# Kernel optimization log

Measured on AMD Instinct MI355X. Metric: run time of the kernel, lower is better.

The kernel has to match this reference:

```python
import jax, jax.numpy as jnp
import numpy as np

B, S, E, H = 2, 2048, 1024, 16
D = E // H  # head dim = 64
NEG_INF = -1e30


def alibi_slopes(n_head):
    # standard ALiBi slopes: 2^(-8*i/n_head), i = 1..n_head
    return jnp.asarray([2.0 ** (-8.0 * (i + 1) / n_head) for i in range(n_head)], dtype=jnp.float32)


def setup_inputs() -> dict:
    key = jax.random.key(0)
    ks = jax.random.split(key, 5)
    scale = 0.02
    return {
        "x": jax.random.normal(ks[0], (B, S, E), dtype=jnp.float32),
        "W_kqv": jax.random.normal(ks[1], (E, 3 * E), dtype=jnp.float32) * scale,
        "b_kqv": jnp.zeros((3 * E,), dtype=jnp.float32),
        "W_proj": jax.random.normal(ks[2], (E, E), dtype=jnp.float32) * scale,
        "b_proj": jnp.zeros((E,), dtype=jnp.float32),
        "slopes": alibi_slopes(H),
    }


def reference(x, W_kqv, b_kqv, W_proj, b_proj, slopes):
    b, s, e = x.shape
    kqv = x @ W_kqv + b_kqv                       # [b, s, 3e]
    k, q, v = jnp.split(kqv, 3, axis=-1)          # split order: k, q, v
    k = k.reshape(b, s, H, D)
    q = q.reshape(b, s, H, D)
    v = v.reshape(b, s, H, D)
    attn = jnp.einsum("bqhd,bkhd->bhqk", q, k) * (1.0 / jnp.sqrt(jnp.float32(D)))
    # ALiBi bias: slope_h * (j - i) for j <= i, -inf above diagonal (causal)
    i = jnp.arange(s)[:, None]
    j = jnp.arange(s)[None, :]
    rel = (j - i).astype(jnp.float32)             # [s, s]
    bias = slopes[:, None, None] * jnp.tril(rel)  # [h, s, s]
    bias = jnp.where(j > i, NEG_INF, bias)
    attn = jax.nn.softmax(attn + bias[None], axis=-1)
    # dropout is identity in eval mode
    y = jnp.einsum("bhqk,bkhd->bqhd", attn, v).reshape(b, s, e)
    return y @ W_proj + b_proj
```

## Files before the change

kernel.cpp:

```cpp
#include <hip/hip_runtime.h>

typedef unsigned short u16;
typedef float f32x4 __attribute__((ext_vector_type(4)));
typedef __bf16 bfx8 __attribute__((ext_vector_type(8)));
typedef __bf16 bfx4 __attribute__((ext_vector_type(4)));
typedef u16 u16x8 __attribute__((ext_vector_type(8)));
typedef u16 u16x4 __attribute__((ext_vector_type(4)));

#define B_ 2
#define S_ 2048
#define E_ 1024
#define H_ 16
#define D_ 64

__device__ __forceinline__ u16 f2bf(float f) {
  unsigned u = __float_as_uint(f);
  u = u + 0x7FFFu + ((u >> 16) & 1u);
  return (u16)(u >> 16);
}

__device__ __forceinline__ int swz128(int o) { return o ^ ((o >> 3) & 0x70); }

__device__ __forceinline__ void gload16(const void* g, void* l) {
  __builtin_amdgcn_global_load_lds((const __attribute__((address_space(1))) void*)g,
                                   (__attribute__((address_space(3))) void*)l, 16, 0, 0);
}

__device__ const signed char TQI[60] = {31, 31, 30, 30, 29, 29, 28, 28, 27, 27, 26, 26, 25, 25, 24,
                                        24, 23, 23, 22, 21, 20, 19, 18, 17, 16, 15, 14, 13, 12, 11,
                                        22, 10, 21, 9,  20, 8,  31, 19, 7,  30, 18, 6,  29, 17, 5,
                                        28, 16, 4,  27, 15, 3,  26, 14, 2,  25, 13, 1,  24, 12, 0};
__device__ const signed char TT0[60] = {0,  12, 0,  12, 0,  12, 0,  12, 0,  12, 0,  12, 0,  12, 0,
                                        12, 0,  12, 0,  0,  0,  0,  0,  0,  0,  0,  0,  0,  0,  0,
                                        12, 0,  12, 0,  12, 0,  24, 12, 0,  24, 12, 0,  24, 12, 0,
                                        24, 12, 0,  24, 12, 0,  24, 12, 0,  24, 12, 0,  24, 12, 0};
__device__ const signed char TT1[60] = {12, 24, 12, 24, 12, 24, 12, 24, 12, 24, 12, 24, 12, 24, 12,
                                        24, 12, 24, 12, 12, 12, 12, 12, 12, 12, 12, 12, 12, 12, 12,
                                        23, 11, 22, 10, 21, 9,  32, 20, 8,  31, 19, 7,  30, 18, 6,
                                        29, 17, 5,  28, 16, 4,  27, 15, 3,  26, 14, 2,  25, 13, 1};
__device__ const signed char TSL[60] = {45, 46, 42, 43, 39, 40, 36, 37, 33, 34, 30, 31, 27, 28, 24,
                                        25, 22, 23, 20, 18, 16, 14, 12, 10, 8,  6,  4,  2,  0,  -1,
                                        21, -1, 19, -1, 17, -1, 47, 15, -1, 44, 13, -1, 41, 11, -1,
                                        38, 9,  -1, 35, 7,  -1, 32, 5,  -1, 29, 3,  -1, 26, 1,  -1};

__global__ __launch_bounds__(256) void prep(const float* __restrict__ x,
                                            const float* __restrict__ Wk,
                                            const float* __restrict__ Wp, u16* __restrict__ xb,
                                            u16* __restrict__ wkt, u16* __restrict__ wpt) {
  __shared__ float tile[64][65];
  const int id = blockIdx.x, tid = threadIdx.x;
  if (id < 2048) {
    const float4* in4 = reinterpret_cast<const float4*>(x);
    u16x4* out4 = reinterpret_cast<u16x4*>(xb);
    int i = id * 256 + tid;
#pragma unroll
    for (int p = 0; p < 2; ++p, i += 524288) {
      const float4 v = in4[i];
      u16x4 o = {f2bf(v.x), f2bf(v.y), f2bf(v.z), f2bf(v.w)};
      out4[i] = o;
    }
    return;
  }
  const float* in;
  u16* out;
  int R, C, bx, by;
  if (id < 2816) {
    const int t = id - 2048;
    in = Wk; out = wkt; R = 1024; C = 3072; bx = t % 48; by = t / 48;
  } else {
    const int t = id - 2816;
    in = Wp; out = wpt; R = 1024; C = 1024; bx = t & 15; by = t >> 4;
  }
  const int ct = bx * 64, rt = by * 64;
#pragma unroll
  for (int p = 0; p < 4; ++p) {
    int f = p * 256 + tid;
    int row = f >> 4, c4 = (f & 15) << 2;
    const float4 v = *reinterpret_cast<const float4*>(in + (size_t)(rt + row) * C + ct + c4);
    tile[row][c4 + 0] = v.x; tile[row][c4 + 1] = v.y;
    tile[row][c4 + 2] = v.z; tile[row][c4 + 3] = v.w;
  }
  __syncthreads();
#pragma unroll
  for (int p = 0; p < 4; ++p) {
    int g = p * 256 + tid;
    int orow = g >> 4, k4 = (g & 15) << 2;
    u16x4 o = {f2bf(tile[k4 + 0][orow]), f2bf(tile[k4 + 1][orow]),
               f2bf(tile[k4 + 2][orow]), f2bf(tile[k4 + 3][orow])};
    *reinterpret_cast<u16x4*>(out + (size_t)(ct + orow) * R + rt + k4) = o;
  }
}

__global__ __launch_bounds__(256) void gemm_kqv(const u16* __restrict__ A,
                                                const u16* __restrict__ Bt,
                                                const float* __restrict__ bias, int M, int N, int K,
                                                u16* __restrict__ outK, u16* __restrict__ outQ,
                                                u16* __restrict__ outVt) {
  __shared__ __align__(16) u16 sA[128 * 64];
  __shared__ __align__(16) u16 sB[128 * 64];
  const int tid = threadIdx.x, lane = tid & 63;
  const int wave = tid >> 6, wr = wave >> 1, wc = wave & 1;
  int lin = blockIdx.y * gridDim.x + blockIdx.x;
  const int nwg = gridDim.x * gridDim.y;
  if ((nwg & 7) == 0) {
    const int cpx = nwg >> 3;
    lin = (lin & 7) * cpx + (lin >> 3);
  }
  const int bm = (lin / gridDim.x) * 128, bn = (lin % gridDim.x) * 128;
  const int r8 = lane >> 3, c16 = (lane & 7) ^ r8;
  f32x4 acc[4][4] = {};
  for (int k0 = 0; k0 < K; k0 += 64) {
#pragma unroll
    for (int i = 0; i < 4; ++i) {
      const int c = wave * 4 + i;
      const int row = c * 8 + r8;
      gload16(A + (size_t)(bm + row) * K + k0 + c16 * 8, (char*)sA + c * 1024);
      gload16(Bt + (size_t)(bn + row) * K + k0 + c16 * 8, (char*)sB + c * 1024);
    }
    __syncthreads();
#pragma unroll
    for (int kc = 0; kc < 2; ++kc) {
      bfx8 af[4], bf[4];
#pragma unroll
      for (int mf = 0; mf < 4; ++mf) {
        int o = swz128(((wr * 64 + mf * 16 + (lane & 15)) << 7) + kc * 64 + ((lane >> 4) << 4));
        af[mf] = *reinterpret_cast<const bfx8*>(reinterpret_cast<const char*>(sA) + o);
      }
#pragma unroll
      for (int nf = 0; nf < 4; ++nf) {
        int o = swz128(((wc * 64 + nf * 16 + (lane & 15)) << 7) + kc * 64 + ((lane >> 4) << 4));
        bf[nf] = *reinterpret_cast<const bfx8*>(reinterpret_cast<const char*>(sB) + o);
      }
#pragma unroll
      for (int mf = 0; mf < 4; ++mf)
#pragma unroll
        for (int nf = 0; nf < 4; ++nf)
          acc[mf][nf] = __builtin_amdgcn_mfma_f32_16x16x32_bf16(af[mf], bf[nf], acc[mf][nf], 0, 0, 0);
    }
    __syncthreads();
  }
#pragma unroll
  for (int mf = 0; mf < 4; ++mf)
#pragma unroll
    for (int nf = 0; nf < 4; ++nf)
#pragma unroll
      for (int r = 0; r < 4; ++r) {
        const int row = bm + wr * 64 + mf * 16 + ((lane >> 4) << 2) + r;
        const int col = bn + wc * 64 + nf * 16 + (lane & 15);
        const float v = acc[mf][nf][r] + bias[col];
        const int chunk = col >> 10, w = col & 1023, h = w >> 6, dd = w & 63;
        const int b = row >> 11, s = row & 2047;
        const int bh = b * H_ + h;
        if (chunk == 0)
          outK[((size_t)bh * S_ + s) * D_ + dd] = f2bf(v);
        else if (chunk == 1)
          outQ[((size_t)bh * S_ + s) * D_ + dd] = f2bf(v);
        else
          outVt[((size_t)bh * D_ + dd) * S_ + s] = f2bf(v);
      }
}

__global__ __launch_bounds__(512) void gemm_proj(const u16* __restrict__ A,
                                                 const u16* __restrict__ Bt,
                                                 const float* __restrict__ bias, int M, int N,
                                                 int K, float* __restrict__ outF) {
  __shared__ __align__(16) u16 sA[128 * 64];
  __shared__ __align__(16) u16 sB[128 * 64];
  const int tid = threadIdx.x, lane = tid & 63;
  const int wave = tid >> 6, wr = wave >> 2, wc = wave & 3;
  int lin = blockIdx.y * gridDim.x + blockIdx.x;
  const int nwg = gridDim.x * gridDim.y;
  if ((nwg & 7) == 0) {
    const int cpx = nwg >> 3;
    lin = (lin & 7) * cpx + (lin >> 3);
  }
  const int bm = (lin / gridDim.x) * 128, bn = (lin % gridDim.x) * 128;
  const int r8 = lane >> 3, c16 = (lane & 7) ^ r8;
  f32x4 acc[4][2] = {};
  for (int k0 = 0; k0 < K; k0 += 64) {
#pragma unroll
    for (int i = 0; i < 2; ++i) {
      const int c = wave * 2 + i;
      const int row = c * 8 + r8;
      gload16(A + (size_t)(bm + row) * K + k0 + c16 * 8, (char*)sA + c * 1024);
      gload16(Bt + (size_t)(bn + row) * K + k0 + c16 * 8, (char*)sB + c * 1024);
    }
    __syncthreads();
#pragma unroll
    for (int kc = 0; kc < 2; ++kc) {
      bfx8 af[4], bf[2];
#pragma unroll
      for (int mf = 0; mf < 4; ++mf) {
        int o = swz128(((wr * 64 + mf * 16 + (lane & 15)) << 7) + kc * 64 + ((lane >> 4) << 4));
        af[mf] = *reinterpret_cast<const bfx8*>(reinterpret_cast<const char*>(sA) + o);
      }
#pragma unroll
      for (int nf = 0; nf < 2; ++nf) {
        int o = swz128(((wc * 32 + nf * 16 + (lane & 15)) << 7) + kc * 64 + ((lane >> 4) << 4));
        bf[nf] = *reinterpret_cast<const bfx8*>(reinterpret_cast<const char*>(sB) + o);
      }
#pragma unroll
      for (int mf = 0; mf < 4; ++mf)
#pragma unroll
        for (int nf = 0; nf < 2; ++nf)
          acc[mf][nf] = __builtin_amdgcn_mfma_f32_16x16x32_bf16(af[mf], bf[nf], acc[mf][nf], 0, 0, 0);
    }
    __syncthreads();
  }
#pragma unroll
  for (int mf = 0; mf < 4; ++mf)
#pragma unroll
    for (int nf = 0; nf < 2; ++nf)
#pragma unroll
      for (int r = 0; r < 4; ++r) {
        const int row = bm + wr * 64 + mf * 16 + ((lane >> 4) << 2) + r;
        const int col = bn + wc * 32 + nf * 16 + (lane & 15);
        outF[(size_t)row * N + col] = acc[mf][nf][r] + bias[col];
      }
}

__global__ __launch_bounds__(256, 4) void attn_alibi(const u16* __restrict__ Q,
                                                     const u16* __restrict__ Kb,
                                                     const u16* __restrict__ Vt,
                                                     const float* __restrict__ slopes,
                                                     u16* __restrict__ Y, u16* __restrict__ pO,
                                                     float* __restrict__ pML) {
  __shared__ __align__(16) u16 sK[2][4096];
  __shared__ __align__(16) u16 sV[2][4096];
  __shared__ __align__(16) __bf16 sP[4][16 * 64];
  const int id = blockIdx.x;
  const int xcd = id & 7, j = id >> 3;
  const int bh = xcd * 4 + (j & 3);
  const int c = j >> 2;
  const int qi = TQI[c], t0 = TT0[c], t1 = TT1[c], slot = TSL[c];
  const int b = bh >> 4, h = bh & 15;
  const int tid = threadIdx.x, lane = tid & 63, wave = tid >> 6;
  const int q = lane & 15, g = lane >> 4;
  const int q0 = qi * 64;
  const int w0 = q0 + wave * 16;
  const float L2E = 1.44269504089f;
  const float SCALE = 0.125f * L2E;
  const float sl2 = slopes[h] * L2E;
  const size_t headSD = (size_t)bh * (S_ * D_);
  const size_t headDS = (size_t)bh * (D_ * S_);
  const int r8 = lane >> 3, c16 = (lane & 7) ^ r8;

  bfx8 qf[2];
  {
    const u16* qp = Q + headSD + (size_t)(w0 + q) * D_ + g * 8;
    qf[0] = *reinterpret_cast<const bfx8*>(qp);
    qf[1] = *reinterpret_cast<const bfx8*>(qp + 32);
  }
  bfx8 onesf;
#pragma unroll
  for (int jj = 0; jj < 8; ++jj) onesf[jj] = (__bf16)1.0f;
  f32x4 base[4];
#pragma unroll
  for (int nf = 0; nf < 4; ++nf)
#pragma unroll
    for (int r = 0; r < 4; ++r) base[nf][r] = sl2 * (float)(nf * 16 + 4 * g + r);
  const int ir0 = wave * 16 + q;

  float m = 0.f;
  f32x4 oT[4] = {};
  f32x4 oX = {};

  auto stage = [&](int t, int buf) {
#pragma unroll
    for (int i = 0; i < 2; ++i) {
      const int cc = wave * 2 + i;
      const int row = cc * 8 + r8;
      gload16(Kb + headSD + (size_t)t * 4096 + row * 64 + c16 * 8, (char*)sK[buf] + cc * 1024);
      gload16(Vt + headDS + (size_t)row * S_ + t * 64 + c16 * 8, (char*)sV[buf] + cc * 1024);
    }
  };

  stage(t0, 0);
  __syncthreads();
  int cur = 0;
  for (int t = t0; t < t1; ++t) {
    if (t + 1 < t1) stage(t + 1, cur ^ 1);
    const char* sKc = reinterpret_cast<const char*>(sK[cur]);
    const char* sVc = reinterpret_cast<const char*>(sV[cur]);
    f32x4 tt[4] = {};
    __builtin_amdgcn_s_setprio(1);
#pragma unroll
    for (int kc = 0; kc < 2; ++kc)
#pragma unroll
      for (int nf = 0; nf < 4; ++nf) {
        const bfx8 kf =
            *reinterpret_cast<const bfx8*>(sKc + swz128(((nf * 16 + q) << 7) + kc * 64 + (g << 4)));
        tt[nf] = __builtin_amdgcn_mfma_f32_16x16x32_bf16(kf, qf[kc], tt[nf], 0, 0, 0);
      }
    __builtin_amdgcn_s_setprio(0);
    const float tb = sl2 * (float)(t * 64);
    if (t != qi) {
      float rmax = -3.0e38f;
#pragma unroll
      for (int nf = 0; nf < 4; ++nf)
#pragma unroll
        for (int r = 0; r < 4; ++r) rmax = fmaxf(rmax, tt[nf][r]);
      rmax = fmaxf(rmax, __shfl_xor(rmax, 16));
      rmax = fmaxf(rmax, __shfl_xor(rmax, 32));
      const float bound = fmaf(rmax, SCALE, tb + sl2 * 63.f);
      if (!__all(bound <= m + 12.0f)) {
        const float mnew = fmaxf(m, bound);
        const float corr = __builtin_amdgcn_exp2f(m - mnew);
        m = mnew;
#pragma unroll
        for (int nf = 0; nf < 4; ++nf) oT[nf] *= corr;
        oX *= corr;
      }
      const float tbm = tb - m;
#pragma unroll
      for (int nf = 0; nf < 4; ++nf) {
        const f32x4 bb = base[nf] + tbm;
#pragma unroll
        for (int r = 0; r < 4; ++r)
          tt[nf][r] = __builtin_amdgcn_exp2f(fmaf(tt[nf][r], SCALE, bb[r]));
      }
    } else {
      float rmax = -3.0e38f;
#pragma unroll
      for (int nf = 0; nf < 4; ++nf)
#pragma unroll
        for (int r = 0; r < 4; ++r) {
          float sv = fmaf(tt[nf][r], SCALE, base[nf][r] + tb);
          if (nf * 16 + 4 * g + r > ir0) sv = -3.0e38f;
          tt[nf][r] = sv;
          rmax = fmaxf(rmax, sv);
        }
      rmax = fmaxf(rmax, __shfl_xor(rmax, 16));
      rmax = fmaxf(rmax, __shfl_xor(rmax, 32));
      if (!__all(rmax <= m + 12.0f)) {
        const float mnew = fmaxf(m, rmax);
        const float corr = __builtin_amdgcn_exp2f(m - mnew);
        m = mnew;
#pragma unroll
        for (int nf = 0; nf < 4; ++nf) oT[nf] *= corr;
        oX *= corr;
      }
#pragma unroll
      for (int nf = 0; nf < 4; ++nf)
#pragma unroll
        for (int r = 0; r < 4; ++r) tt[nf][r] = __builtin_amdgcn_exp2f(tt[nf][r] - m);
    }
    char* pw = reinterpret_cast<char*>(sP[wave]);
#pragma unroll
    for (int nf = 0; nf < 4; ++nf) {
      bfx4 w = {(__bf16)tt[nf][0], (__bf16)tt[nf][1], (__bf16)tt[nf][2], (__bf16)tt[nf][3]};
      *reinterpret_cast<bfx4*>(pw + swz128((q << 7) + nf * 32 + g * 8)) = w;
    }
    bfx8 pa[2];
#pragma unroll
    for (int kc = 0; kc < 2; ++kc)
      pa[kc] = *reinterpret_cast<const bfx8*>(pw + swz128((q << 7) + kc * 64 + (g << 4)));
    __builtin_amdgcn_s_setprio(1);
#pragma unroll
    for (int kc = 0; kc < 2; ++kc) {
#pragma unroll
      for (int nf = 0; nf < 4; ++nf) {
        const bfx8 vf =
            *reinterpret_cast<const bfx8*>(sVc + swz128(((nf * 16 + q) << 7) + kc * 64 + (g << 4)));
        oT[nf] = __builtin_amdgcn_mfma_f32_16x16x32_bf16(vf, pa[kc], oT[nf], 0, 0, 0);
      }
      oX = __builtin_amdgcn_mfma_f32_16x16x32_bf16(onesf, pa[kc], oX, 0, 0, 0);
    }
    __builtin_amdgcn_s_setprio(0);
    __syncthreads();
    cur ^= 1;
  }
  if (slot < 0) {
    const float rl = 1.0f / oX[0];
    const int row = w0 + q;
#pragma unroll
    for (int nf = 0; nf < 4; ++nf) {
      bfx4 w = {(__bf16)(oT[nf][0] * rl), (__bf16)(oT[nf][1] * rl), (__bf16)(oT[nf][2] * rl),
                (__bf16)(oT[nf][3] * rl)};
      const int col = h * 64 + nf * 16 + g * 4;
      *reinterpret_cast<bfx4*>(reinterpret_cast<char*>(Y) +
                               (((size_t)b * S_ + row) * E_ + col) * 2) = w;
    }
  } else {
    const int sg = bh * 48 + slot;
    u16* po = pO + (size_t)sg * 4096 + (size_t)(wave * 16 + q) * 64;
#pragma unroll
    for (int nf = 0; nf < 4; ++nf) {
      bfx4 w = {(__bf16)oT[nf][0], (__bf16)oT[nf][1], (__bf16)oT[nf][2], (__bf16)oT[nf][3]};
      *reinterpret_cast<bfx4*>(po + nf * 16 + g * 4) = w;
    }
    if (g == 0) {
      float2 ml = make_float2(m, oX[0]);
      reinterpret_cast<float2*>(pML)[sg * 64 + wave * 16 + q] = ml;
    }
  }
}

__global__ __launch_bounds__(256) void merge_attn(const u16* __restrict__ pO,
                                                  const float* __restrict__ pML,
                                                  u16* __restrict__ Y) {
  const int mb = blockIdx.x;
  const int bh = mb / 20, qq = mb % 20, qi = 12 + qq;
  const int nch = (qi < 24) ? 2 : 3;
  const int sb = (qi < 24) ? (qi - 12) * 2 : 24 + (qi - 24) * 3;
  const int b = bh >> 4, h = bh & 15;
  const int tid = threadIdx.x;
  const int r = tid >> 2, dq = (tid & 3) * 16;
  const float2* ml2 = reinterpret_cast<const float2*>(pML);
  float mm[3], ll[3];
  float M = -3.0e38f;
#pragma unroll
  for (int c = 0; c < 3; ++c) {
    if (c < nch) {
      const float2 v = ml2[(bh * 48 + sb + c) * 64 + r];
      mm[c] = v.x;
      ll[c] = v.y;
      M = fmaxf(M, v.x);
    } else {
      mm[c] = -3.0e38f;
      ll[c] = 0.f;
    }
  }
  float L = 0.f, acc[16];
#pragma unroll
  for (int i = 0; i < 16; ++i) acc[i] = 0.f;
#pragma unroll
  for (int c = 0; c < 3; ++c) {
    if (c < nch) {
      const float w = __builtin_amdgcn_exp2f(mm[c] - M);
      L += w * ll[c];
      const u16* src = pO + (size_t)(bh * 48 + sb + c) * 4096 + r * 64 + dq;
      const u16x8 a = *reinterpret_cast<const u16x8*>(src);
      const u16x8 bb = *reinterpret_cast<const u16x8*>(src + 8);
#pragma unroll
      for (int i = 0; i < 8; ++i) {
        acc[i] += w * __uint_as_float(((unsigned)a[i]) << 16);
        acc[8 + i] += w * __uint_as_float(((unsigned)bb[i]) << 16);
      }
    }
  }
  const float rl = 1.0f / L;
  u16x8 o0, o1;
#pragma unroll
  for (int i = 0; i < 8; ++i) {
    o0[i] = f2bf(acc[i] * rl);
    o1[i] = f2bf(acc[8 + i] * rl);
  }
  u16* dst = Y + ((size_t)b * S_ + qi * 64 + r) * E_ + h * 64 + dq;
  *reinterpret_cast<u16x8*>(dst) = o0;
  *reinterpret_cast<u16x8*>(dst + 8) = o1;
}

extern "C" void kernel_launch(void* const* d_in, const int* in_sizes, int n_in, void* d_out,
                              int out_size, void* d_ws, size_t ws_size, hipStream_t stream) {
  (void)in_sizes; (void)n_in; (void)out_size; (void)ws_size;
  const float* x = (const float*)d_in[0];
  const float* Wkqv = (const float*)d_in[1];
  const float* bkqv = (const float*)d_in[2];
  const float* Wproj = (const float*)d_in[3];
  const float* bproj = (const float*)d_in[4];
  const float* slopes = (const float*)d_in[5];
  float* out = (float*)d_out;

  const size_t MBE = (size_t)4096 * 1024;
  u16* xb = (u16*)d_ws;
  u16* wkqvt = xb + MBE;
  u16* wprojt = wkqvt + (size_t)3072 * 1024;
  u16* kbuf = wprojt + (size_t)1024 * 1024;
  u16* qbuf = kbuf + MBE;
  u16* vtbuf = qbuf + MBE;
  u16* ybuf = vtbuf + MBE;
  u16* pO = xb;
  float* pML = (float*)(xb + (size_t)1536 * 4096);

  prep<<<dim3(3072), dim3(256), 0, stream>>>(x, Wkqv, Wproj, xb, wkqvt, wprojt);
  gemm_kqv<<<dim3(24, 32), dim3(256), 0, stream>>>(xb, wkqvt, bkqv, 4096, 3072, 1024, kbuf, qbuf,
                                                   vtbuf);
  attn_alibi<<<dim3(1920), dim3(256), 0, stream>>>(qbuf, kbuf, vtbuf, slopes, ybuf, pO, pML);
  merge_attn<<<dim3(640), dim3(256), 0, stream>>>(pO, pML, ybuf);
  gemm_proj<<<dim3(8, 32), dim3(512), 0, stream>>>(ybuf, wprojt, bproj, 4096, 1024, 1024, out);
}
```

Before: 115.0 us.

## Stage KQV epilogue through LDS for vector stores; double-buffer proj GEMM

The KQV GEMM epilogue now writes bias-added bf16 results into padded shared memory, transposing them for the V chunk, then emits coalesced 16-byte stores to K, Q and Vt. This replaces scattered 2-byte stores, which were especially strided for the transposed V output. Separately, the projection GEMM double-buffers its LDS tiles so the next K-slice load is issued while the current one is computed. The cost is more LDS per block, which may lower occupancy, plus an extra barrier in the epilogue.

```diff
diff --git a/kernel.cpp b/kernel.cpp
--- a/kernel.cpp
+++ b/kernel.cpp
@@ -96,8 +96,9 @@
                                                 const float* __restrict__ bias, int M, int N, int K,
                                                 u16* __restrict__ outK, u16* __restrict__ outQ,
                                                 u16* __restrict__ outVt) {
-  __shared__ __align__(16) u16 sA[128 * 64];
-  __shared__ __align__(16) u16 sB[128 * 64];
+  __shared__ __align__(16) u16 smem[17408];
+  u16* sA = smem;
+  u16* sB = smem + 8192;
   const int tid = threadIdx.x, lane = tid & 63;
   const int wave = tid >> 6, wr = wave >> 1, wc = wave & 1;
   int lin = blockIdx.y * gridDim.x + blockIdx.x;
@@ -139,33 +140,57 @@
     }
     __syncthreads();
   }
-#pragma unroll
-  for (int mf = 0; mf < 4; ++mf)
-#pragma unroll
-    for (int nf = 0; nf < 4; ++nf)
-#pragma unroll
-      for (int r = 0; r < 4; ++r) {
-        const int row = bm + wr * 64 + mf * 16 + ((lane >> 4) << 2) + r;
-        const int col = bn + wc * 64 + nf * 16 + (lane & 15);
-        const float v = acc[mf][nf][r] + bias[col];
-        const int chunk = col >> 10, w = col & 1023, h = w >> 6, dd = w & 63;
-        const int b = row >> 11, s = row & 2047;
-        const int bh = b * H_ + h;
-        if (chunk == 0)
-          outK[((size_t)bh * S_ + s) * D_ + dd] = f2bf(v);
-        else if (chunk == 1)
-          outQ[((size_t)bh * S_ + s) * D_ + dd] = f2bf(v);
-        else
-          outVt[((size_t)bh * D_ + dd) * S_ + s] = f2bf(v);
-      }
+  const int chunk = bn >> 10;
+  const int g4 = lane >> 4, c15 = lane & 15;
+  if (chunk < 2) {
+#pragma unroll
+    for (int mf = 0; mf < 4; ++mf)
+#pragma unroll
+      for (int nf = 0; nf < 4; ++nf) {
+        const int col = wc * 64 + nf * 16 + c15;
+        const float bs = bias[bn + col];
+#pragma unroll
+        for (int r = 0; r < 4; ++r)
+          smem[(wr * 64 + mf * 16 + g4 * 4 + r) * 136 + col] = f2bf(acc[mf][nf][r] + bs);
+      }
+  } else {
+#pragma unroll
+    for (int mf = 0; mf < 4; ++mf)
+#pragma unroll
+      for (int nf = 0; nf < 4; ++nf) {
+        const int col = wc * 64 + nf * 16 + c15;
+        const float bs = bias[bn + col];
+        bfx4 w = {(__bf16)(acc[mf][nf][0] + bs), (__bf16)(acc[mf][nf][1] + bs),
+                  (__bf16)(acc[mf][nf][2] + bs), (__bf16)(acc[mf][nf][3] + bs)};
+        *reinterpret_cast<bfx4*>(smem + col * 136 + wr * 64 + mf * 16 + g4 * 4) = w;
+      }
+  }
+  __syncthreads();
+  const int bloc = bm >> 11, srow0 = bm & 2047;
+#pragma unroll
+  for (int p = 0; p < 8; ++p) {
+    const int idx = p * 256 + tid;
+    const int row = idx >> 4, cq = (idx & 15) * 8;
+    const u16x8 v = *reinterpret_cast<const u16x8*>(smem + row * 136 + cq);
+    if (chunk < 2) {
+      const int h = ((bn & 1023) >> 6) + (cq >> 6);
+      u16* dst = ((chunk == 0) ? outK : outQ) +
+                 (((size_t)(bloc * H_ + h)) * S_ + srow0 + row) * D_ + (cq & 63);
+      *reinterpret_cast<u16x8*>(dst) = v;
+    } else {
+      const int h = ((bn & 1023) >> 6) + (row >> 6);
+      u16* dst = outVt + (((size_t)(bloc * H_ + h)) * D_ + (row & 63)) * S_ + srow0 + cq;
+      *reinterpret_cast<u16x8*>(dst) = v;
+    }
+  }
 }
 
 __global__ __launch_bounds__(512) void gemm_proj(const u16* __restrict__ A,
                                                  const u16* __restrict__ Bt,
                                                  const float* __restrict__ bias, int M, int N,
                                                  int K, float* __restrict__ outF) {
-  __shared__ __align__(16) u16 sA[128 * 64];
-  __shared__ __align__(16) u16 sB[128 * 64];
+  __shared__ __align__(16) u16 sA[2][8192];
+  __shared__ __align__(16) u16 sB[2][8192];
   const int tid = threadIdx.x, lane = tid & 63;
   const int wave = tid >> 6, wr = wave >> 2, wc = wave & 3;
   int lin = blockIdx.y * gridDim.x + blockIdx.x;
@@ -177,27 +202,34 @@
   const int bm = (lin / gridDim.x) * 128, bn = (lin % gridDim.x) * 128;
   const int r8 = lane >> 3, c16 = (lane & 7) ^ r8;
   f32x4 acc[4][2] = {};
-  for (int k0 = 0; k0 < K; k0 += 64) {
+
+  auto stage = [&](int k0, int buf) {
 #pragma unroll
     for (int i = 0; i < 2; ++i) {
       const int c = wave * 2 + i;
       const int row = c * 8 + r8;
-      gload16(A + (size_t)(bm + row) * K + k0 + c16 * 8, (char*)sA + c * 1024);
-      gload16(Bt + (size_t)(bn + row) * K + k0 + c16 * 8, (char*)sB + c * 1024);
-    }
-    __syncthreads();
+      gload16(A + (size_t)(bm + row) * K + k0 + c16 * 8, (char*)sA[buf] + c * 1024);
+      gload16(Bt + (size_t)(bn + row) * K + k0 + c16 * 8, (char*)sB[buf] + c * 1024);
+    }
+  };
+
+  stage(0, 0);
+  __syncthreads();
+  int cur = 0;
+  for (int k0 = 0; k0 < K; k0 += 64) {
+    if (k0 + 64 < K) stage(k0 + 64, cur ^ 1);
 #pragma unroll
     for (int kc = 0; kc < 2; ++kc) {
       bfx8 af[4], bf[2];
 #pragma unroll
       for (int mf = 0; mf < 4; ++mf) {
         int o = swz128(((wr * 64 + mf * 16 + (lane & 15)) << 7) + kc * 64 + ((lane >> 4) << 4));
-        af[mf] = *reinterpret_cast<const bfx8*>(reinterpret_cast<const char*>(sA) + o);
+        af[mf] = *reinterpret_cast<const bfx8*>(reinterpret_cast<const char*>(sA[cur]) + o);
       }
 #pragma unroll
       for (int nf = 0; nf < 2; ++nf) {
         int o = swz128(((wc * 32 + nf * 16 + (lane & 15)) << 7) + kc * 64 + ((lane >> 4) << 4));
-        bf[nf] = *reinterpret_cast<const bfx8*>(reinterpret_cast<const char*>(sB) + o);
+        bf[nf] = *reinterpret_cast<const bfx8*>(reinterpret_cast<const char*>(sB[cur]) + o);
       }
 #pragma unroll
       for (int mf = 0; mf < 4; ++mf)
@@ -206,6 +238,7 @@
           acc[mf][nf] = __builtin_amdgcn_mfma_f32_16x16x32_bf16(af[mf], bf[nf], acc[mf][nf], 0, 0, 0);
     }
     __syncthreads();
+    cur ^= 1;
   }
 #pragma unroll
   for (int mf = 0; mf < 4; ++mf)
```

Result: slower. 117.5 us (+2.1%).
